# Optimization experiments

Hardware: AMD Instinct MI355X
Metric: run time of the kernel (lower is better)

## Reference

```python
import jax, jax.numpy as jnp
import numpy as np

N = 50000
IN_DIM = 1024
HID = 64
HEADS = 4
OUT_DIM = 128
NEG_SLOPE = 0.2


def setup_inputs() -> dict:
    key = jax.random.key(0)
    ks = jax.random.split(key, 10)
    x = jax.random.normal(ks[0], (N, IN_DIM), dtype=jnp.float32)
    edge_index = jax.random.randint(ks[1], (2, 800000), 0, N, dtype=jnp.int64)
    # GATConv 1: input_dim -> hidden_dim, heads=HEADS, concat=True
    W1 = jax.random.normal(ks[2], (IN_DIM, HEADS * HID), dtype=jnp.float32) * (1.0 / np.sqrt(IN_DIM))
    att_src1 = jax.random.normal(ks[3], (HEADS, HID), dtype=jnp.float32) * 0.1
    att_dst1 = jax.random.normal(ks[4], (HEADS, HID), dtype=jnp.float32) * 0.1
    b1 = jnp.zeros((HEADS * HID,), dtype=jnp.float32)
    # GATConv 2: hidden_dim*heads -> output_dim, heads=1, concat=False
    W2 = jax.random.normal(ks[5], (HEADS * HID, OUT_DIM), dtype=jnp.float32) * (1.0 / np.sqrt(HEADS * HID))
    att_src2 = jax.random.normal(ks[6], (1, OUT_DIM), dtype=jnp.float32) * 0.1
    att_dst2 = jax.random.normal(ks[7], (1, OUT_DIM), dtype=jnp.float32) * 0.1
    b2 = jnp.zeros((OUT_DIM,), dtype=jnp.float32)
    return {"x": x, "edge_index": edge_index, "W1": W1, "att_src1": att_src1,
            "att_dst1": att_dst1, "b1": b1, "W2": W2, "att_src2": att_src2,
            "att_dst2": att_dst2, "b2": b2}


def _gat_conv(x, src, dst, W, a_src, a_dst, b, heads, concat):
    # x: [N, F_in]; src/dst: [E'] (self-loops already included)
    n = x.shape[0]
    h = (x @ W).reshape(n, heads, -1)                 # [N, H, D]
    # per-node attention halves (PyG style)
    alpha_s = jnp.sum(h * a_src[None], axis=-1)       # [N, H]
    alpha_d = jnp.sum(h * a_dst[None], axis=-1)       # [N, H]
    e = jax.nn.leaky_relu(alpha_s[src] + alpha_d[dst], NEG_SLOPE)  # [E', H]
    # segment softmax over incoming edges of each destination node
    m = jax.ops.segment_max(e, dst, num_segments=n)   # [N, H]
    m = jnp.where(jnp.isfinite(m), m, 0.0)
    e = jnp.exp(e - m[dst])
    s = jax.ops.segment_sum(e, dst, num_segments=n)   # [N, H]
    alpha = e / (s[dst] + 1e-16)                      # [E', H]
    out = jax.ops.segment_sum(h[src] * alpha[:, :, None], dst, num_segments=n)  # [N, H, D]
    out = out.reshape(n, -1) if concat else out.mean(axis=1)
    return out + b


def reference(x, edge_index, W1, att_src1, att_dst1, b1, W2, att_src2, att_dst2, b2):
    n = x.shape[0]
    # PyG GATConv default: add self-loops
    loops = jnp.arange(n, dtype=edge_index.dtype)
    src = jnp.concatenate([edge_index[0], loops])
    dst = jnp.concatenate([edge_index[1], loops])
    # dropout layers are identity in eval mode
    h = _gat_conv(x, src, dst, W1, att_src1, att_dst1, b1, HEADS, concat=True)
    h = jax.nn.elu(h)
    out = _gat_conv(h, src, dst, W2, att_src2, att_dst2, b2, 1, concat=False)
    # F.normalize(p=2, dim=-1)
    norm = jnp.maximum(jnp.linalg.norm(out, axis=-1, keepdims=True), 1e-12)
    return out / norm
```

## Files before the change

kernel.cpp:

```cpp
#include <hip/hip_runtime.h>
#include <math.h>

#define NNODES 50000
#define E0 800000
#define ETOT 850000
#define IN_DIM 1024
#define HEADS 4
#define C1 256
#define C2 128
#define NEG_SLOPE 0.2f

typedef short bf16x8 __attribute__((ext_vector_type(8)));
typedef float f32x4 __attribute__((ext_vector_type(4)));
typedef unsigned short ushort_t;

__device__ __forceinline__ void edge_sd(const int* __restrict__ ei, int e, int& s, int& d) {
    if (e < E0) { s = ei[e]; d = ei[E0 + e]; }
    else        { s = e - E0; d = s; }
}

__device__ __forceinline__ ushort_t f2b(float f) {
    unsigned u = __float_as_uint(f);
    return (ushort_t)((u + 0x7fffu + ((u >> 16) & 1u)) >> 16);
}
__device__ __forceinline__ float bf2f(ushort_t u) {
    return __uint_as_float((unsigned)u << 16);
}
__device__ __forceinline__ float lrelu(float v) { return v > 0.f ? v : NEG_SLOPE * v; }

__device__ __forceinline__ bf16x8 cvt_bf8(float4 f0, float4 f1) {
    bf16x8 p;
    p[0] = f2b(f0.x); p[1] = f2b(f0.y); p[2] = f2b(f0.z); p[3] = f2b(f0.w);
    p[4] = f2b(f1.x); p[5] = f2b(f1.y); p[6] = f2b(f1.z); p[7] = f2b(f1.w);
    return p;
}

__global__ __launch_bounds__(256) void wtrans_kernel(const float* __restrict__ W,
                                                     ushort_t* __restrict__ WT,
                                                     int K, int N)
{
    int idx = blockIdx.x * 256 + threadIdx.x;
    if (idx >= K * N) return;
    int k = idx / N, n = idx % N;
    WT[((size_t)(k >> 3) * N + n) * 8 + (k & 7)] = f2b(W[idx]);
}

__global__ __launch_bounds__(256, 4) void gemm_fb(const float* __restrict__ A,
                                                  const ushort_t* __restrict__ Bblk,
                                                  ushort_t* __restrict__ Cb,
                                                  int M, int N, int K)
{
    const int tid  = threadIdx.x;
    const int lane = tid & 63;
    const int wid  = tid >> 6;
    const int rowBase = blockIdx.x * 128 + wid * 32;
    const int colBase = blockIdx.y * 64;
    const int r0 = lane & 15;
    const int kh = lane >> 4;

    const float* aP0 = A + (size_t)min(rowBase + r0,      M - 1) * K + kh * 8;
    const float* aP1 = A + (size_t)min(rowBase + 16 + r0, M - 1) * K + kh * 8;
    const ushort_t* bP = Bblk + ((size_t)kh * N + colBase + r0) * 8;
    const size_t bStep = (size_t)4 * N * 8;

    f32x4 zero = {0.f, 0.f, 0.f, 0.f};
    f32x4 acc[2][4];
    #pragma unroll
    for (int i = 0; i < 2; ++i)
        #pragma unroll
        for (int j = 0; j < 4; ++j) acc[i][j] = zero;

    float4 sa[4], sb[4];
    sa[0] = *(const float4*)(aP0 + 0); sa[1] = *(const float4*)(aP0 + 4);
    sa[2] = *(const float4*)(aP1 + 0); sa[3] = *(const float4*)(aP1 + 4);

    const int nt = K >> 5;
    for (int t = 0; t < nt; t += 2) {
        {
            const int kt1 = (t + 1) << 5;
            sb[0] = *(const float4*)(aP0 + kt1 + 0); sb[1] = *(const float4*)(aP0 + kt1 + 4);
            sb[2] = *(const float4*)(aP1 + kt1 + 0); sb[3] = *(const float4*)(aP1 + kt1 + 4);
            const ushort_t* bb = bP + (size_t)t * bStep;
            bf16x8 bF[4];
            #pragma unroll
            for (int fj = 0; fj < 4; ++fj) bF[fj] = *(const bf16x8*)(bb + fj * 128);
            bf16x8 aF0 = cvt_bf8(sa[0], sa[1]);
            bf16x8 aF1 = cvt_bf8(sa[2], sa[3]);
            #pragma unroll
            for (int fj = 0; fj < 4; ++fj) {
                acc[0][fj] = __builtin_amdgcn_mfma_f32_16x16x32_bf16(aF0, bF[fj], acc[0][fj], 0, 0, 0);
                acc[1][fj] = __builtin_amdgcn_mfma_f32_16x16x32_bf16(aF1, bF[fj], acc[1][fj], 0, 0, 0);
            }
        }
        {
            const bool has2 = (t + 2) < nt;
            if (has2) {
                const int kt2 = (t + 2) << 5;
                sa[0] = *(const float4*)(aP0 + kt2 + 0); sa[1] = *(const float4*)(aP0 + kt2 + 4);
                sa[2] = *(const float4*)(aP1 + kt2 + 0); sa[3] = *(const float4*)(aP1 + kt2 + 4);
            }
            const ushort_t* bb = bP + (size_t)(t + 1) * bStep;
            bf16x8 bF[4];
            #pragma unroll
            for (int fj = 0; fj < 4; ++fj) bF[fj] = *(const bf16x8*)(bb + fj * 128);
            bf16x8 aF0 = cvt_bf8(sb[0], sb[1]);
            bf16x8 aF1 = cvt_bf8(sb[2], sb[3]);
            #pragma unroll
            for (int fj = 0; fj < 4; ++fj) {
                acc[0][fj] = __builtin_amdgcn_mfma_f32_16x16x32_bf16(aF0, bF[fj], acc[0][fj], 0, 0, 0);
                acc[1][fj] = __builtin_amdgcn_mfma_f32_16x16x32_bf16(aF1, bF[fj], acc[1][fj], 0, 0, 0);
            }
        }
    }

    #pragma unroll
    for (int fi = 0; fi < 2; ++fi) {
        int row0 = rowBase + fi * 16 + kh * 4;
        #pragma unroll
        for (int i = 0; i < 4; ++i) {
            int row = row0 + i;
            if (row < M) {
                #pragma unroll
                for (int fj = 0; fj < 4; ++fj)
                    Cb[(size_t)row * N + colBase + fj * 16 + r0] = f2b(acc[fi][fj][i]);
            }
        }
    }
}

__global__ __launch_bounds__(256, 4) void gemm_bb(const ushort_t* __restrict__ Ab,
                                                  const ushort_t* __restrict__ Bblk,
                                                  ushort_t* __restrict__ Cb,
                                                  int M, int N, int K)
{
    const int tid  = threadIdx.x;
    const int lane = tid & 63;
    const int wid  = tid >> 6;
    const int rowBase = blockIdx.x * 128 + wid * 32;
    const int colBase = blockIdx.y * 64;
    const int r0 = lane & 15;
    const int kh = lane >> 4;

    const ushort_t* aP0 = Ab + (size_t)min(rowBase + r0,      M - 1) * K + kh * 8;
    const ushort_t* aP1 = Ab + (size_t)min(rowBase + 16 + r0, M - 1) * K + kh * 8;
    const ushort_t* bP = Bblk + ((size_t)kh * N + colBase + r0) * 8;
    const size_t bStep = (size_t)4 * N * 8;

    f32x4 zero = {0.f, 0.f, 0.f, 0.f};
    f32x4 acc[2][4];
    #pragma unroll
    for (int i = 0; i < 2; ++i)
        #pragma unroll
        for (int j = 0; j < 4; ++j) acc[i][j] = zero;

    bf16x8 sa0, sa1, sb0, sb1;
    sa0 = *(const bf16x8*)(aP0); sa1 = *(const bf16x8*)(aP1);

    const int nt = K >> 5;
    for (int t = 0; t < nt; t += 2) {
        {
            const int kt1 = (t + 1) << 5;
            sb0 = *(const bf16x8*)(aP0 + kt1); sb1 = *(const bf16x8*)(aP1 + kt1);
            const ushort_t* bb = bP + (size_t)t * bStep;
            bf16x8 bF[4];
            #pragma unroll
            for (int fj = 0; fj < 4; ++fj) bF[fj] = *(const bf16x8*)(bb + fj * 128);
            #pragma unroll
            for (int fj = 0; fj < 4; ++fj) {
                acc[0][fj] = __builtin_amdgcn_mfma_f32_16x16x32_bf16(sa0, bF[fj], acc[0][fj], 0, 0, 0);
                acc[1][fj] = __builtin_amdgcn_mfma_f32_16x16x32_bf16(sa1, bF[fj], acc[1][fj], 0, 0, 0);
            }
        }
        {
            const bool has2 = (t + 2) < nt;
            if (has2) {
                const int kt2 = (t + 2) << 5;
                sa0 = *(const bf16x8*)(aP0 + kt2); sa1 = *(const bf16x8*)(aP1 + kt2);
            }
            const ushort_t* bb = bP + (size_t)(t + 1) * bStep;
            bf16x8 bF[4];
            #pragma unroll
            for (int fj = 0; fj < 4; ++fj) bF[fj] = *(const bf16x8*)(bb + fj * 128);
            #pragma unroll
            for (int fj = 0; fj < 4; ++fj) {
                acc[0][fj] = __builtin_amdgcn_mfma_f32_16x16x32_bf16(sb0, bF[fj], acc[0][fj], 0, 0, 0);
                acc[1][fj] = __builtin_amdgcn_mfma_f32_16x16x32_bf16(sb1, bF[fj], acc[1][fj], 0, 0, 0);
            }
        }
    }

    #pragma unroll
    for (int fi = 0; fi < 2; ++fi) {
        int row0 = rowBase + fi * 16 + kh * 4;
        #pragma unroll
        for (int i = 0; i < 4; ++i) {
            int row = row0 + i;
            if (row < M) {
                #pragma unroll
                for (int fj = 0; fj < 4; ++fj)
                    Cb[(size_t)row * N + colBase + fj * 16 + r0] = f2b(acc[fi][fj][i]);
            }
        }
    }
}

__global__ __launch_bounds__(256) void alpha1_kernel(const ushort_t* __restrict__ h1b,
                                                     const float* __restrict__ asrc,
                                                     const float* __restrict__ adst,
                                                     float* __restrict__ out_s,
                                                     float* __restrict__ out_d)
{
    int n = blockIdx.x;
    int t = threadIdx.x;
    float h = bf2f(h1b[(size_t)n * C1 + t]);
    float s = h * asrc[t];
    float d = h * adst[t];
    #pragma unroll
    for (int off = 32; off > 0; off >>= 1) {
        s += __shfl_down(s, off);
        d += __shfl_down(d, off);
    }
    if ((t & 63) == 0) {
        out_s[n * HEADS + (t >> 6)] = s;
        out_d[n * HEADS + (t >> 6)] = d;
    }
}

__global__ __launch_bounds__(64) void alpha2_kernel(const ushort_t* __restrict__ h2b,
                                                    const float* __restrict__ asrc,
                                                    const float* __restrict__ adst,
                                                    float* __restrict__ out_s,
                                                    float* __restrict__ out_d)
{
    int n = blockIdx.x;
    int t = threadIdx.x;
    float a = bf2f(h2b[(size_t)n * C2 + t]);
    float b = bf2f(h2b[(size_t)n * C2 + t + 64]);
    float s = a * asrc[t] + b * asrc[t + 64];
    float d = a * adst[t] + b * adst[t + 64];
    #pragma unroll
    for (int off = 32; off > 0; off >>= 1) {
        s += __shfl_down(s, off);
        d += __shfl_down(d, off);
    }
    if (t == 0) { out_s[n] = s; out_d[n] = d; }
}

__global__ __launch_bounds__(256) void deg_kernel(const int* __restrict__ ei,
                                                  int* __restrict__ deg)
{
    int e = blockIdx.x * blockDim.x + threadIdx.x;
    if (e >= ETOT) return;
    int s, d; edge_sd(ei, e, s, d);
    atomicAdd(&deg[d], 1);
}

#define SCAN_T 1024
__global__ __launch_bounds__(SCAN_T) void scan_kernel(const int* __restrict__ deg,
                                                      int* __restrict__ rowptr)
{
    __shared__ int wsum[16];
    __shared__ int chunk_tot;
    __shared__ int carry_s;
    const int t = threadIdx.x, lane = t & 63, w = t >> 6;
    if (t == 0) carry_s = 0;
    __syncthreads();
    for (int base = 0; base < NNODES; base += SCAN_T * 4) {
        int idx = base + t * 4;
        int v0 = (idx + 0 < NNODES) ? deg[idx + 0] : 0;
        int v1 = (idx + 1 < NNODES) ? deg[idx + 1] : 0;
        int v2 = (idx + 2 < NNODES) ? deg[idx + 2] : 0;
        int v3 = (idx + 3 < NNODES) ? deg[idx + 3] : 0;
        int p0 = v0, p1 = p0 + v1, p2 = p1 + v2, p3 = p2 + v3;
        int incl = p3;
        #pragma unroll
        for (int off = 1; off < 64; off <<= 1) {
            int nb = __shfl_up(incl, off);
            if (lane >= off) incl += nb;
        }
        if (lane == 63) wsum[w] = incl;
        __syncthreads();
        if (w == 0 && lane < 16) {
            int ws = wsum[lane];
            int wincl = ws;
            #pragma unroll
            for (int off = 1; off < 16; off <<= 1) {
                int nb = __shfl_up(wincl, off);
                if (lane >= off) wincl += nb;
            }
            wsum[lane] = wincl - ws;
            if (lane == 15) chunk_tot = wincl;
        }
        __syncthreads();
        int carry = carry_s;
        int basev = carry + wsum[w] + (incl - p3);
        if (idx + 0 < NNODES) rowptr[idx + 0] = basev;
        if (idx + 1 < NNODES) rowptr[idx + 1] = basev + p0;
        if (idx + 2 < NNODES) rowptr[idx + 2] = basev + p1;
        if (idx + 3 < NNODES) rowptr[idx + 3] = basev + p2;
        __syncthreads();
        if (t == 0) carry_s = carry + chunk_tot;
        __syncthreads();
    }
    if (threadIdx.x == 0) rowptr[NNODES] = carry_s;
}

__global__ __launch_bounds__(256) void scatter_kernel(const int* __restrict__ ei,
                                                      int* __restrict__ cursor,
                                                      int* __restrict__ srcs)
{
    int e = blockIdx.x * blockDim.x + threadIdx.x;
    if (e >= ETOT) return;
    int s, d; edge_sd(ei, e, s, d);
    int pos = atomicAdd(&cursor[d], 1);
    srcs[pos] = s;
}

__global__ __launch_bounds__(256) void weights1_kernel(const int* __restrict__ rowptr,
                                                       const int* __restrict__ srcs,
                                                       const float4* __restrict__ as1,
                                                       const float4* __restrict__ ad1,
                                                       float4* __restrict__ wbuf)
{
    int d = blockIdx.x * 4 + (threadIdx.x >> 6);
    if (d >= NNODES) return;
    int lane = threadIdx.x & 63;
    int beg = rowptr[d], end = rowptr[d + 1];
    float4 adv = ad1[d];
    float m0 = -INFINITY, m1 = -INFINITY, m2 = -INFINITY, m3 = -INFINITY;
    for (int i = beg + lane; i < end; i += 64) {
        int s = srcs[i];
        float4 av = as1[s];
        m0 = fmaxf(m0, lrelu(av.x + adv.x));
        m1 = fmaxf(m1, lrelu(av.y + adv.y));
        m2 = fmaxf(m2, lrelu(av.z + adv.z));
        m3 = fmaxf(m3, lrelu(av.w + adv.w));
    }
    #pragma unroll
    for (int off = 32; off > 0; off >>= 1) {
        m0 = fmaxf(m0, __shfl_xor(m0, off));
        m1 = fmaxf(m1, __shfl_xor(m1, off));
        m2 = fmaxf(m2, __shfl_xor(m2, off));
        m3 = fmaxf(m3, __shfl_xor(m3, off));
    }
    float s0 = 0.f, s1 = 0.f, s2 = 0.f, s3 = 0.f;
    for (int i = beg + lane; i < end; i += 64) {
        int s = srcs[i];
        float4 av = as1[s];
        float w0 = expf(lrelu(av.x + adv.x) - m0);
        float w1 = expf(lrelu(av.y + adv.y) - m1);
        float w2 = expf(lrelu(av.z + adv.z) - m2);
        float w3 = expf(lrelu(av.w + adv.w) - m3);
        wbuf[i] = make_float4(w0, w1, w2, w3);
        s0 += w0; s1 += w1; s2 += w2; s3 += w3;
    }
    #pragma unroll
    for (int off = 32; off > 0; off >>= 1) {
        s0 += __shfl_xor(s0, off);
        s1 += __shfl_xor(s1, off);
        s2 += __shfl_xor(s2, off);
        s3 += __shfl_xor(s3, off);
    }
    float i0 = 1.f / (s0 + 1e-16f), i1 = 1.f / (s1 + 1e-16f);
    float i2 = 1.f / (s2 + 1e-16f), i3 = 1.f / (s3 + 1e-16f);
    for (int i = beg + lane; i < end; i += 64) {
        float4 wv = wbuf[i];
        wbuf[i] = make_float4(wv.x * i0, wv.y * i1, wv.z * i2, wv.w * i3);
    }
}

__global__ __launch_bounds__(256) void weights2_kernel(const int* __restrict__ rowptr,
                                                       const int* __restrict__ srcs,
                                                       const float* __restrict__ as2,
                                                       const float* __restrict__ ad2,
                                                       float* __restrict__ wbuf)
{
    int d = blockIdx.x * 4 + (threadIdx.x >> 6);
    if (d >= NNODES) return;
    int lane = threadIdx.x & 63;
    int beg = rowptr[d], end = rowptr[d + 1];
    float adv = ad2[d];
    float m = -INFINITY;
    for (int i = beg + lane; i < end; i += 64)
        m = fmaxf(m, lrelu(as2[srcs[i]] + adv));
    #pragma unroll
    for (int off = 32; off > 0; off >>= 1) m = fmaxf(m, __shfl_xor(m, off));
    float sm = 0.f;
    for (int i = beg + lane; i < end; i += 64) {
        float w = expf(lrelu(as2[srcs[i]] + adv) - m);
        wbuf[i] = w;
        sm += w;
    }
    #pragma unroll
    for (int off = 32; off > 0; off >>= 1) sm += __shfl_xor(sm, off);
    float inv = 1.f / (sm + 1e-16f);
    for (int i = beg + lane; i < end; i += 64) wbuf[i] *= inv;
}

__global__ __launch_bounds__(256) void aggr1_csr(const int* __restrict__ rowptr,
                                                 const int* __restrict__ srcs,
                                                 const ushort_t* __restrict__ h1b,
                                                 const float* __restrict__ wbuf,
                                                 const float* __restrict__ b1,
                                                 ushort_t* __restrict__ out)
{
    int d = blockIdx.x * 4 + (threadIdx.x >> 6);
    if (d >= NNODES) return;
    int lane = threadIdx.x & 63;
    int c0 = lane * 4;
    int head = lane >> 4;
    int beg = rowptr[d], end = rowptr[d + 1];
    float a0 = 0.f, a1 = 0.f, a2 = 0.f, a3 = 0.f;
    int i = beg;
    for (; i + 3 < end; i += 4) {
        int s0 = srcs[i], s1 = srcs[i + 1], s2 = srcs[i + 2], s3 = srcs[i + 3];
        float w0 = wbuf[i * 4 + head],     w1 = wbuf[i * 4 + 4 + head];
        float w2 = wbuf[i * 4 + 8 + head], w3 = wbuf[i * 4 + 12 + head];
        ushort4 v0 = *(const ushort4*)(h1b + (size_t)s0 * C1 + c0);
        ushort4 v1 = *(const ushort4*)(h1b + (size_t)s1 * C1 + c0);
        ushort4 v2 = *(const ushort4*)(h1b + (size_t)s2 * C1 + c0);
        ushort4 v3 = *(const ushort4*)(h1b + (size_t)s3 * C1 + c0);
        a0 = fmaf(w0, bf2f(v0.x), a0); a1 = fmaf(w0, bf2f(v0.y), a1);
        a2 = fmaf(w0, bf2f(v0.z), a2); a3 = fmaf(w0, bf2f(v0.w), a3);
        a0 = fmaf(w1, bf2f(v1.x), a0); a1 = fmaf(w1, bf2f(v1.y), a1);
        a2 = fmaf(w1, bf2f(v1.z), a2); a3 = fmaf(w1, bf2f(v1.w), a3);
        a0 = fmaf(w2, bf2f(v2.x), a0); a1 = fmaf(w2, bf2f(v2.y), a1);
        a2 = fmaf(w2, bf2f(v2.z), a2); a3 = fmaf(w2, bf2f(v2.w), a3);
        a0 = fmaf(w3, bf2f(v3.x), a0); a1 = fmaf(w3, bf2f(v3.y), a1);
        a2 = fmaf(w3, bf2f(v3.z), a2); a3 = fmaf(w3, bf2f(v3.w), a3);
    }
    for (; i < end; ++i) {
        int s0 = srcs[i];
        float w0 = wbuf[i * 4 + head];
        ushort4 v0 = *(const ushort4*)(h1b + (size_t)s0 * C1 + c0);
        a0 = fmaf(w0, bf2f(v0.x), a0); a1 = fmaf(w0, bf2f(v0.y), a1);
        a2 = fmaf(w0, bf2f(v0.z), a2); a3 = fmaf(w0, bf2f(v0.w), a3);
    }
    float4 bv = *(const float4*)(b1 + c0);
    float o0 = a0 + bv.x, o1 = a1 + bv.y, o2 = a2 + bv.z, o3 = a3 + bv.w;
    ushort4 r;
    r.x = f2b(o0 > 0.f ? o0 : (expf(o0) - 1.f));
    r.y = f2b(o1 > 0.f ? o1 : (expf(o1) - 1.f));
    r.z = f2b(o2 > 0.f ? o2 : (expf(o2) - 1.f));
    r.w = f2b(o3 > 0.f ? o3 : (expf(o3) - 1.f));
    *(ushort4*)(out + (size_t)d * C1 + c0) = r;
}

__global__ __launch_bounds__(256) void aggr2_csr(const int* __restrict__ rowptr,
                                                 const int* __restrict__ srcs,
                                                 const ushort_t* __restrict__ h2b,
                                                 const float* __restrict__ wbuf,
                                                 const float* __restrict__ b2,
                                                 float* __restrict__ out)
{
    int d = blockIdx.x * 4 + (threadIdx.x >> 6);
    if (d >= NNODES) return;
    int lane = threadIdx.x & 63;
    int c0 = lane * 2;
    int beg = rowptr[d], end = rowptr[d + 1];
    float a0 = 0.f, a1 = 0.f;
    int i = beg;
    for (; i + 3 < end; i += 4) {
        int s0 = srcs[i], s1 = srcs[i + 1], s2 = srcs[i + 2], s3 = srcs[i + 3];
        float w0 = wbuf[i], w1 = wbuf[i + 1], w2 = wbuf[i + 2], w3 = wbuf[i + 3];
        ushort2 v0 = *(const ushort2*)(h2b + (size_t)s0 * C2 + c0);
        ushort2 v1 = *(const ushort2*)(h2b + (size_t)s1 * C2 + c0);
        ushort2 v2 = *(const ushort2*)(h2b + (size_t)s2 * C2 + c0);
        ushort2 v3 = *(const ushort2*)(h2b + (size_t)s3 * C2 + c0);
        a0 = fmaf(w0, bf2f(v0.x), a0); a1 = fmaf(w0, bf2f(v0.y), a1);
        a0 = fmaf(w1, bf2f(v1.x), a0); a1 = fmaf(w1, bf2f(v1.y), a1);
        a0 = fmaf(w2, bf2f(v2.x), a0); a1 = fmaf(w2, bf2f(v2.y), a1);
        a0 = fmaf(w3, bf2f(v3.x), a0); a1 = fmaf(w3, bf2f(v3.y), a1);
    }
    for (; i < end; ++i) {
        float w0 = wbuf[i];
        ushort2 v0 = *(const ushort2*)(h2b + (size_t)srcs[i] * C2 + c0);
        a0 = fmaf(w0, bf2f(v0.x), a0); a1 = fmaf(w0, bf2f(v0.y), a1);
    }
    float2 bv = *(const float2*)(b2 + c0);
    float o0 = a0 + bv.x, o1 = a1 + bv.y;
    float sq = o0 * o0 + o1 * o1;
    #pragma unroll
    for (int off = 32; off > 0; off >>= 1) sq += __shfl_xor(sq, off);
    float inv = 1.0f / fmaxf(sqrtf(sq), 1e-12f);
    float2 r = make_float2(o0 * inv, o1 * inv);
    *(float2*)(out + (size_t)d * C2 + c0) = r;
}

extern "C" void kernel_launch(void* const* d_in, const int* in_sizes, int n_in,
                              void* d_out, int out_size, void* d_ws, size_t ws_size,
                              hipStream_t stream)
{
    const float* x     = (const float*)d_in[0];
    const int*   ei    = (const int*)d_in[1];
    const float* W1    = (const float*)d_in[2];
    const float* asrc1 = (const float*)d_in[3];
    const float* adst1 = (const float*)d_in[4];
    const float* b1    = (const float*)d_in[5];
    const float* W2    = (const float*)d_in[6];
    const float* asrc2 = (const float*)d_in[7];
    const float* adst2 = (const float*)d_in[8];
    const float* b2    = (const float*)d_in[9];
    float* out = (float*)d_out;

    char* ws = (char*)d_ws;
    size_t off = 0;
    auto alloc = [&](size_t nbytes) {
        void* p = ws + off;
        off += (nbytes + 15) & ~(size_t)15;
        return p;
    };
    ushort_t* h1b    = (ushort_t*)alloc((size_t)NNODES * C1 * 2);
    ushort_t* act1b  = (ushort_t*)alloc((size_t)NNODES * C1 * 2);
    ushort_t* h2b    = (ushort_t*)alloc((size_t)NNODES * C2 * 2);
    ushort_t* W1blk  = (ushort_t*)alloc((size_t)C1 * IN_DIM * 2);
    ushort_t* W2blk  = (ushort_t*)alloc((size_t)C2 * C1 * 2);
    float*    as1    = (float*)alloc((size_t)NNODES * HEADS * 4);
    float*    ad1    = (float*)alloc((size_t)NNODES * HEADS * 4);
    float*    as2    = (float*)alloc((size_t)NNODES * 4);
    float*    ad2    = (float*)alloc((size_t)NNODES * 4);
    float*    wbuf1  = (float*)alloc((size_t)ETOT * HEADS * 4);
    float*    wbuf2  = (float*)alloc((size_t)ETOT * 4);
    int*      deg    = (int*)alloc((size_t)NNODES * 4);
    int*      rowptr = (int*)alloc((size_t)(NNODES + 1) * 4);
    int*      cursor = (int*)alloc((size_t)(NNODES + 1) * 4);
    int*      srcs   = (int*)alloc((size_t)ETOT * 4);

    const int eb = (ETOT + 255) / 256;
    const int nb4 = (NNODES + 3) / 4;
    const int rb = (NNODES + 127) / 128;

    wtrans_kernel<<<(IN_DIM * C1 + 255) / 256, 256, 0, stream>>>(W1, W1blk, IN_DIM, C1);
    wtrans_kernel<<<(C1 * C2 + 255) / 256, 256, 0, stream>>>(W2, W2blk, C1, C2);

    hipMemsetAsync(deg, 0, (size_t)NNODES * 4, stream);
    deg_kernel<<<eb, 256, 0, stream>>>(ei, deg);
    scan_kernel<<<1, SCAN_T, 0, stream>>>(deg, rowptr);
    hipMemcpyAsync(cursor, rowptr, (size_t)(NNODES + 1) * 4, hipMemcpyDeviceToDevice, stream);
    scatter_kernel<<<eb, 256, 0, stream>>>(ei, cursor, srcs);

    dim3 g1(rb, C1 / 64);
    gemm_fb<<<g1, 256, 0, stream>>>(x, W1blk, h1b, NNODES, C1, IN_DIM);
    alpha1_kernel<<<NNODES, 256, 0, stream>>>(h1b, asrc1, adst1, as1, ad1);
    weights1_kernel<<<nb4, 256, 0, stream>>>(rowptr, srcs, (const float4*)as1,
                                             (const float4*)ad1, (float4*)wbuf1);
    aggr1_csr<<<nb4, 256, 0, stream>>>(rowptr, srcs, h1b, wbuf1, b1, act1b);

    dim3 g2(rb, C2 / 64);
    gemm_bb<<<g2, 256, 0, stream>>>(act1b, W2blk, h2b, NNODES, C2, C1);
    alpha2_kernel<<<NNODES, 64, 0, stream>>>(h2b, asrc2, adst2, as2, ad2);
    weights2_kernel<<<nb4, 256, 0, stream>>>(rowptr, srcs, as2, ad2, wbuf2);
    aggr2_csr<<<nb4, 256, 0, stream>>>(rowptr, srcs, h2b, wbuf2, b2, out);
}
```

Measured before the change: 480.3 us.

## Widen GEMM column tile to 128 and put column blocks on the fast grid axis

Both MFMA GEMMs now compute 128 columns per block instead of 64, doubling the accumulators per wave. Each A fragment (fp32 x converted to bf16 in layer 1) is therefore loaded and converted once per row block instead of twice. The grid is reordered so column tiles are the fast-varying dimension, which lets neighbouring blocks share A rows in cache. In exchange it raises register pressure (launch bounds drop from 4 to 3 blocks per CU), halves the block count, and loads B fragments inside the MFMA loop, which can reduce latency hiding.

```diff
diff --git a/kernel.cpp b/kernel.cpp
--- a/kernel.cpp
+++ b/kernel.cpp
@@ -45,7 +45,7 @@
     WT[((size_t)(k >> 3) * N + n) * 8 + (k & 7)] = f2b(W[idx]);
 }
 
-__global__ __launch_bounds__(256, 4) void gemm_fb(const float* __restrict__ A,
+__global__ __launch_bounds__(256, 3) void gemm_fb(const float* __restrict__ A,
                                                   const ushort_t* __restrict__ Bblk,
                                                   ushort_t* __restrict__ Cb,
                                                   int M, int N, int K)
@@ -53,8 +53,8 @@
     const int tid  = threadIdx.x;
     const int lane = tid & 63;
     const int wid  = tid >> 6;
-    const int rowBase = blockIdx.x * 128 + wid * 32;
-    const int colBase = blockIdx.y * 64;
+    const int rowBase = blockIdx.y * 128 + wid * 32;
+    const int colBase = blockIdx.x * 128;
     const int r0 = lane & 15;
     const int kh = lane >> 4;
 
@@ -64,11 +64,11 @@
     const size_t bStep = (size_t)4 * N * 8;
 
     f32x4 zero = {0.f, 0.f, 0.f, 0.f};
-    f32x4 acc[2][4];
+    f32x4 acc[2][8];
     #pragma unroll
     for (int i = 0; i < 2; ++i)
         #pragma unroll
-        for (int j = 0; j < 4; ++j) acc[i][j] = zero;
+        for (int j = 0; j < 8; ++j) acc[i][j] = zero;
 
     float4 sa[4], sb[4];
     sa[0] = *(const float4*)(aP0 + 0); sa[1] = *(const float4*)(aP0 + 4);
@@ -81,15 +81,13 @@
             sb[0] = *(const float4*)(aP0 + kt1 + 0); sb[1] = *(const float4*)(aP0 + kt1 + 4);
             sb[2] = *(const float4*)(aP1 + kt1 + 0); sb[3] = *(const float4*)(aP1 + kt1 + 4);
             const ushort_t* bb = bP + (size_t)t * bStep;
-            bf16x8 bF[4];
-            #pragma unroll
-            for (int fj = 0; fj < 4; ++fj) bF[fj] = *(const bf16x8*)(bb + fj * 128);
             bf16x8 aF0 = cvt_bf8(sa[0], sa[1]);
             bf16x8 aF1 = cvt_bf8(sa[2], sa[3]);
             #pragma unroll
-            for (int fj = 0; fj < 4; ++fj) {
-                acc[0][fj] = __builtin_amdgcn_mfma_f32_16x16x32_bf16(aF0, bF[fj], acc[0][fj], 0, 0, 0);
-                acc[1][fj] = __builtin_amdgcn_mfma_f32_16x16x32_bf16(aF1, bF[fj], acc[1][fj], 0, 0, 0);
+            for (int fj = 0; fj < 8; ++fj) {
+                bf16x8 bF = *(const bf16x8*)(bb + fj * 128);
+                acc[0][fj] = __builtin_amdgcn_mfma_f32_16x16x32_bf16(aF0, bF, acc[0][fj], 0, 0, 0);
+                acc[1][fj] = __builtin_amdgcn_mfma_f32_16x16x32_bf16(aF1, bF, acc[1][fj], 0, 0, 0);
             }
         }
         {
@@ -100,15 +98,13 @@
                 sa[2] = *(const float4*)(aP1 + kt2 + 0); sa[3] = *(const float4*)(aP1 + kt2 + 4);
             }
             const ushort_t* bb = bP + (size_t)(t + 1) * bStep;
-            bf16x8 bF[4];
-            #pragma unroll
-            for (int fj = 0; fj < 4; ++fj) bF[fj] = *(const bf16x8*)(bb + fj * 128);
             bf16x8 aF0 = cvt_bf8(sb[0], sb[1]);
             bf16x8 aF1 = cvt_bf8(sb[2], sb[3]);
             #pragma unroll
-            for (int fj = 0; fj < 4; ++fj) {
-                acc[0][fj] = __builtin_amdgcn_mfma_f32_16x16x32_bf16(aF0, bF[fj], acc[0][fj], 0, 0, 0);
-                acc[1][fj] = __builtin_amdgcn_mfma_f32_16x16x32_bf16(aF1, bF[fj], acc[1][fj], 0, 0, 0);
+            for (int fj = 0; fj < 8; ++fj) {
+                bf16x8 bF = *(const bf16x8*)(bb + fj * 128);
+                acc[0][fj] = __builtin_amdgcn_mfma_f32_16x16x32_bf16(aF0, bF, acc[0][fj], 0, 0, 0);
+                acc[1][fj] = __builtin_amdgcn_mfma_f32_16x16x32_bf16(aF1, bF, acc[1][fj], 0, 0, 0);
             }
         }
     }
@@ -121,14 +117,14 @@
             int row = row0 + i;
             if (row < M) {
                 #pragma unroll
-                for (int fj = 0; fj < 4; ++fj)
+                for (int fj = 0; fj < 8; ++fj)
                     Cb[(size_t)row * N + colBase + fj * 16 + r0] = f2b(acc[fi][fj][i]);
             }
         }
     }
 }
 
-__global__ __launch_bounds__(256, 4) void gemm_bb(const ushort_t* __restrict__ Ab,
+__global__ __launch_bounds__(256, 3) void gemm_bb(const ushort_t* __restrict__ Ab,
                                                   const ushort_t* __restrict__ Bblk,
                                                   ushort_t* __restrict__ Cb,
                                                   int M, int N, int K)
@@ -136,8 +132,8 @@
     const int tid  = threadIdx.x;
     const int lane = tid & 63;
     const int wid  = tid >> 6;
-    const int rowBase = blockIdx.x * 128 + wid * 32;
-    const int colBase = blockIdx.y * 64;
+    const int rowBase = blockIdx.y * 128 + wid * 32;
+    const int colBase = blockIdx.x * 128;
     const int r0 = lane & 15;
     const int kh = lane >> 4;
 
@@ -147,11 +143,11 @@
     const size_t bStep = (size_t)4 * N * 8;
 
     f32x4 zero = {0.f, 0.f, 0.f, 0.f};
-    f32x4 acc[2][4];
+    f32x4 acc[2][8];
     #pragma unroll
     for (int i = 0; i < 2; ++i)
         #pragma unroll
-        for (int j = 0; j < 4; ++j) acc[i][j] = zero;
+        for (int j = 0; j < 8; ++j) acc[i][j] = zero;
 
     bf16x8 sa0, sa1, sb0, sb1;
     sa0 = *(const bf16x8*)(aP0); sa1 = *(const bf16x8*)(aP1);
@@ -162,13 +158,11 @@
             const int kt1 = (t + 1) << 5;
             sb0 = *(const bf16x8*)(aP0 + kt1); sb1 = *(const bf16x8*)(aP1 + kt1);
             const ushort_t* bb = bP + (size_t)t * bStep;
-            bf16x8 bF[4];
             #pragma unroll
-            for (int fj = 0; fj < 4; ++fj) bF[fj] = *(const bf16x8*)(bb + fj * 128);
-            #pragma unroll
-            for (int fj = 0; fj < 4; ++fj) {
-                acc[0][fj] = __builtin_amdgcn_mfma_f32_16x16x32_bf16(sa0, bF[fj], acc[0][fj], 0, 0, 0);
-                acc[1][fj] = __builtin_amdgcn_mfma_f32_16x16x32_bf16(sa1, bF[fj], acc[1][fj], 0, 0, 0);
+            for (int fj = 0; fj < 8; ++fj) {
+                bf16x8 bF = *(const bf16x8*)(bb + fj * 128);
+                acc[0][fj] = __builtin_amdgcn_mfma_f32_16x16x32_bf16(sa0, bF, acc[0][fj], 0, 0, 0);
+                acc[1][fj] = __builtin_amdgcn_mfma_f32_16x16x32_bf16(sa1, bF, acc[1][fj], 0, 0, 0);
             }
         }
         {
@@ -178,13 +172,11 @@
                 sa0 = *(const bf16x8*)(aP0 + kt2); sa1 = *(const bf16x8*)(aP1 + kt2);
             }
             const ushort_t* bb = bP + (size_t)(t + 1) * bStep;
-            bf16x8 bF[4];
             #pragma unroll
-            for (int fj = 0; fj < 4; ++fj) bF[fj] = *(const bf16x8*)(bb + fj * 128);
-            #pragma unroll
-            for (int fj = 0; fj < 4; ++fj) {
-                acc[0][fj] = __builtin_amdgcn_mfma_f32_16x16x32_bf16(sb0, bF[fj], acc[0][fj], 0, 0, 0);
-                acc[1][fj] = __builtin_amdgcn_mfma_f32_16x16x32_bf16(sb1, bF[fj], acc[1][fj], 0, 0, 0);
+            for (int fj = 0; fj < 8; ++fj) {
+                bf16x8 bF = *(const bf16x8*)(bb + fj * 128);
+                acc[0][fj] = __builtin_amdgcn_mfma_f32_16x16x32_bf16(sb0, bF, acc[0][fj], 0, 0, 0);
+                acc[1][fj] = __builtin_amdgcn_mfma_f32_16x16x32_bf16(sb1, bF, acc[1][fj], 0, 0, 0);
             }
         }
     }
@@ -197,7 +189,7 @@
             int row = row0 + i;
             if (row < M) {
                 #pragma unroll
-                for (int fj = 0; fj < 4; ++fj)
+                for (int fj = 0; fj < 8; ++fj)
                     Cb[(size_t)row * N + colBase + fj * 16 + r0] = f2b(acc[fi][fj][i]);
             }
         }
@@ -539,14 +531,14 @@
     hipMemcpyAsync(cursor, rowptr, (size_t)(NNODES + 1) * 4, hipMemcpyDeviceToDevice, stream);
     scatter_kernel<<<eb, 256, 0, stream>>>(ei, cursor, srcs);
 
-    dim3 g1(rb, C1 / 64);
+    dim3 g1(C1 / 128, rb);
     gemm_fb<<<g1, 256, 0, stream>>>(x, W1blk, h1b, NNODES, C1, IN_DIM);
     alpha1_kernel<<<NNODES, 256, 0, stream>>>(h1b, asrc1, adst1, as1, ad1);
     weights1_kernel<<<nb4, 256, 0, stream>>>(rowptr, srcs, (const float4*)as1,
                                              (const float4*)ad1, (float4*)wbuf1);
     aggr1_csr<<<nb4, 256, 0, stream>>>(rowptr, srcs, h1b, wbuf1, b1, act1b);
 
-    dim3 g2(rb, C2 / 64);
+    dim3 g2(C2 / 128, rb);
     gemm_bb<<<g2, 256, 0, stream>>>(act1b, W2blk, h2b, NNODES, C2, C1);
     alpha2_kernel<<<NNODES, 64, 0, stream>>>(h2b, asrc2, adst2, as2, ad2);
     weights2_kernel<<<nb4, 256, 0, stream>>>(rowptr, srcs, as2, ad2, wbuf2);
```

Measured after the change: 466.4 us (median of 2 runs). -2.9%, faster.
